# Performance work log

Measured on AMD Instinct MI355X. Metric: run time of the kernel, lower is better.

## Reference

```python
import jax, jax.numpy as jnp
import numpy as np

N = 100000
E = 1600000
IN_C = 128
HID = 64
HEADS = 2
OUT_C = 64
Z = 16
NEG_SLOPE = 0.2


def _gat_layer(x, src, dst, W, a_src, a_dst, b, heads, d):
    # x: [N, in], W: [in, heads*d]
    h = (x @ W).reshape(-1, heads, d)                      # [N, H, d]
    alpha_s = (h * a_src).sum(-1)                          # [N, H]
    alpha_d = (h * a_dst).sum(-1)                          # [N, H]
    e = jax.nn.leaky_relu(alpha_s[src] + alpha_d[dst], NEG_SLOPE)  # [E, H]
    m = jax.ops.segment_max(e, dst, num_segments=N)        # [N, H]
    ex = jnp.exp(e - m[dst])
    denom = jax.ops.segment_sum(ex, dst, num_segments=N)   # [N, H]
    alpha = ex / (denom[dst] + 1e-16)                      # [E, H]
    out = jax.ops.segment_sum(h[src] * alpha[:, :, None], dst, num_segments=N)  # [N, H, d]
    return out.reshape(-1, heads * d) + b


def setup_inputs() -> dict:
    key = jax.random.key(0)
    ks = jax.random.split(key, 24)
    g = lambda k, shp, fan: jax.random.normal(k, shp, jnp.float32) * (1.0 / np.sqrt(fan))
    inp = {
        "x": jax.random.normal(ks[0], (N, IN_C), jnp.float32),
        "edge_index": jax.random.randint(ks[1], (2, E), 0, N, jnp.int64),
        "edge_attr": jax.random.normal(ks[2], (E, 8), jnp.float32),
        "eps": jax.random.normal(ks[3], (N, Z), jnp.float32),
        # GAT layer 1: heads=2, d=HID
        "W1": g(ks[4], (IN_C, HEADS * HID), IN_C),
        "a_src1": g(ks[5], (HEADS, HID), HID),
        "a_dst1": g(ks[6], (HEADS, HID), HID),
        "b1": jnp.zeros((HEADS * HID,), jnp.float32),
        # GAT layer 2: heads=1, d=OUT_C
        "W2": g(ks[7], (HEADS * HID, OUT_C), HEADS * HID),
        "a_src2": g(ks[8], (1, OUT_C), OUT_C),
        "a_dst2": g(ks[9], (1, OUT_C), OUT_C),
        "b2": jnp.zeros((OUT_C,), jnp.float32),
        # VAE
        "fc1_w": g(ks[10], (64, 128), 64), "fc1_b": jnp.zeros((128,), jnp.float32),
        "mu_w": g(ks[11], (128, Z), 128), "mu_b": jnp.zeros((Z,), jnp.float32),
        "lv_w": g(ks[12], (128, Z), 128), "lv_b": jnp.zeros((Z,), jnp.float32),
        "fc3_w": g(ks[13], (Z, 128), Z), "fc3_b": jnp.zeros((128,), jnp.float32),
        "fc4_w": g(ks[14], (128, 64), 128), "fc4_b": jnp.zeros((64,), jnp.float32),
    }
    return inp


def reference(x, edge_index, edge_attr, eps, W1, a_src1, a_dst1, b1, W2, a_src2, a_dst2, b2,
              fc1_w, fc1_b, mu_w, mu_b, lv_w, lv_b, fc3_w, fc3_b, fc4_w, fc4_b):
    src, dst = edge_index[0], edge_index[1]
    # GAT stack (edge_attr ignored: GATConv edge_dim=None)
    h = jax.nn.relu(_gat_layer(x, src, dst, W1, a_src1, a_dst1, b1, HEADS, HID))
    gat_out = _gat_layer(h, src, dst, W2, a_src2, a_dst2, b2, 1, OUT_C)  # [N, 64]
    # VAE
    h1 = jax.nn.relu(gat_out @ fc1_w + fc1_b)
    mu = h1 @ mu_w + mu_b
    logvar = h1 @ lv_w + lv_b
    lv = jnp.clip(logvar, -10.0, 10.0)
    z = mu + eps * jnp.exp(0.5 * lv)
    h3 = jax.nn.relu(z @ fc3_w + fc3_b)
    recon = h3 @ fc4_w + fc4_b
    return recon, mu, logvar, gat_out
```

## Files before the change

kernel.cpp:

```cpp
#include <hip/hip_runtime.h>
#include <hip/hip_bf16.h>

__device__ __forceinline__ float4 fma4(float s, float4 b, float4 c) {
    c.x = fmaf(s, b.x, c.x); c.y = fmaf(s, b.y, c.y);
    c.z = fmaf(s, b.z, c.z); c.w = fmaf(s, b.w, c.w);
    return c;
}

__device__ __forceinline__ unsigned short f2b_bits(float x) {
    __hip_bfloat16 h = __float2bfloat16(x);
    unsigned short u;
    __builtin_memcpy(&u, &h, 2);
    return u;
}
__device__ __forceinline__ unsigned int pack2(float a, float b) {
    return (unsigned int)f2b_bits(a) | ((unsigned int)f2b_bits(b) << 16);
}
__device__ __forceinline__ float blo(unsigned int u) { return __uint_as_float(u << 16); }
__device__ __forceinline__ float bhi(unsigned int u) { return __uint_as_float(u & 0xffff0000u); }
__device__ __forceinline__ float sx8(unsigned int w, int b) {
    return (float)((int)(w << (24 - 8 * b)) >> 24);
}

template<int FIN, int FOUT, int BK, int ACT, int OUTK, bool ABF, int HD>
__global__ __launch_bounds__(256) void tgemm_k(const void* __restrict__ Av,
                                               const float* __restrict__ W,
                                               const float* __restrict__ bias,
                                               void* __restrict__ outv,
                                               float* __restrict__ scales,
                                               const float* __restrict__ asr,
                                               const float* __restrict__ adr,
                                               float* __restrict__ aso,
                                               float* __restrict__ ado, int n)
{
    constexpr int BM  = 128;
    constexpr int BMp = BM + 4;
    constexpr int NT_N = FOUT / 4;
    constexpr int NT_M = 256 / NT_N;
    constexpr int RG   = (BM / NT_M) / 4;
    __shared__ __align__(16) float As[BK * BMp];
    __shared__ __align__(16) float Bs[BK * FOUT];

    const float* Af = (const float*)Av;
    const unsigned short* Ab = (const unsigned short*)Av;

    const int t  = threadIdx.x;
    const int m0 = blockIdx.x * BM;
    const int tn = t % NT_N, tm = t / NT_N;

    float4 acc[RG][4];
    #pragma unroll
    for (int g = 0; g < RG; ++g)
        #pragma unroll
        for (int i = 0; i < 4; ++i) acc[g][i] = make_float4(0.f, 0.f, 0.f, 0.f);

    for (int kt = 0; kt < FIN; kt += BK) {
        __syncthreads();
        #pragma unroll
        for (int idx = t; idx < BM * BK / 4; idx += 256) {
            int r  = idx / (BK / 4);
            int c4 = (idx % (BK / 4)) * 4;
            int row = m0 + r;
            float4 v = make_float4(0.f, 0.f, 0.f, 0.f);
            if (row < n) {
                if constexpr (ABF) {
                    uint2 rv = *(const uint2*)(Ab + (size_t)row * FIN + kt + c4);
                    v = make_float4(blo(rv.x), bhi(rv.x), blo(rv.y), bhi(rv.y));
                } else {
                    v = *(const float4*)(Af + (size_t)row * FIN + kt + c4);
                }
            }
            As[(c4 + 0) * BMp + r] = v.x;
            As[(c4 + 1) * BMp + r] = v.y;
            As[(c4 + 2) * BMp + r] = v.z;
            As[(c4 + 3) * BMp + r] = v.w;
        }
        #pragma unroll
        for (int idx = t; idx < BK * FOUT / 4; idx += 256) {
            int kr = idx / (FOUT / 4);
            int c4 = (idx % (FOUT / 4)) * 4;
            *(float4*)(Bs + kr * FOUT + c4) =
                *(const float4*)(W + (size_t)(kt + kr) * FOUT + c4);
        }
        __syncthreads();
        #pragma unroll 8
        for (int k = 0; k < BK; ++k) {
            float4 b = *(const float4*)(Bs + k * FOUT + 4 * tn);
            #pragma unroll
            for (int g = 0; g < RG; ++g) {
                float4 a = *(const float4*)(As + k * BMp + 4 * (tm + NT_M * g));
                acc[g][0] = fma4(a.x, b, acc[g][0]);
                acc[g][1] = fma4(a.y, b, acc[g][1]);
                acc[g][2] = fma4(a.z, b, acc[g][2]);
                acc[g][3] = fma4(a.w, b, acc[g][3]);
            }
        }
    }

    if constexpr (HD > 0) {
        float4 av = *(const float4*)(asr + 4 * tn);
        float4 dv = *(const float4*)(adr + 4 * tn);
        const int head = tn / (NT_N / HD);
        #pragma unroll
        for (int g = 0; g < RG; ++g)
            #pragma unroll
            for (int i = 0; i < 4; ++i) {
                float4 o = acc[g][i];
                float ds = fmaf(o.x, av.x, fmaf(o.y, av.y, fmaf(o.z, av.z, o.w * av.w)));
                float dd = fmaf(o.x, dv.x, fmaf(o.y, dv.y, fmaf(o.z, dv.z, o.w * dv.w)));
                #pragma unroll
                for (int off = 8; off > 0; off >>= 1) {
                    ds += __shfl_xor(ds, off, 16);
                    dd += __shfl_xor(dd, off, 16);
                }
                if ((tn & 15) == 0) {
                    int row = m0 + 4 * (tm + NT_M * g) + i;
                    if (row < n) {
                        aso[(size_t)row * HD + head] = ds;
                        ado[(size_t)row * HD + head] = dd;
                    }
                }
            }
    }

    float4 bb = make_float4(0.f, 0.f, 0.f, 0.f);
    if (bias) bb = *(const float4*)(bias + 4 * tn);
    #pragma unroll
    for (int g = 0; g < RG; ++g)
        #pragma unroll
        for (int i = 0; i < 4; ++i) {
            int row = m0 + 4 * (tm + NT_M * g) + i;
            if (row < n) {
                float4 o = acc[g][i];
                if constexpr (OUTK == 2) {
                    float amax = fmaxf(fmaxf(fabsf(o.x), fabsf(o.y)),
                                       fmaxf(fabsf(o.z), fabsf(o.w)));
                    #pragma unroll
                    for (int off = NT_N / 2; off > 0; off >>= 1)
                        amax = fmaxf(amax, __shfl_xor(amax, off, NT_N));
                    float invsc = amax > 0.f ? 127.f / amax : 0.f;
                    int q0 = __float2int_rn(o.x * invsc);
                    int q1 = __float2int_rn(o.y * invsc);
                    int q2 = __float2int_rn(o.z * invsc);
                    int q3 = __float2int_rn(o.w * invsc);
                    unsigned int pv = (q0 & 255) | ((q1 & 255) << 8) |
                                      ((q2 & 255) << 16) | ((q3 & 255) << 24);
                    ((unsigned int*)outv)[(size_t)row * (FOUT / 4) + tn] = pv;
                    if (tn == 0) scales[row] = amax * (1.f / 127.f);
                } else {
                    o.x += bb.x; o.y += bb.y; o.z += bb.z; o.w += bb.w;
                    if (ACT == 1) {
                        o.x = fmaxf(o.x, 0.f); o.y = fmaxf(o.y, 0.f);
                        o.z = fmaxf(o.z, 0.f); o.w = fmaxf(o.w, 0.f);
                    }
                    if constexpr (OUTK == 1) {
                        unsigned short* outb = (unsigned short*)outv;
                        uint2 pv = make_uint2(pack2(o.x, o.y), pack2(o.z, o.w));
                        *(uint2*)(outb + (size_t)row * FOUT + 4 * tn) = pv;
                    } else {
                        float* outf = (float*)outv;
                        *(float4*)(outf + (size_t)row * FOUT + 4 * tn) = o;
                    }
                }
            }
        }
}

__global__ __launch_bounds__(256) void mulv_k(const float* __restrict__ A,
                                              const float* __restrict__ muw,
                                              const float* __restrict__ lvw,
                                              const float* __restrict__ mub,
                                              const float* __restrict__ lvb,
                                              const float* __restrict__ eps,
                                              float* __restrict__ o_mu,
                                              float* __restrict__ o_lv,
                                              float* __restrict__ zb, int n)
{
    constexpr int FIN = 128, BK = 32, BN = 32;
    constexpr int BM = 128, BMp = BM + 4;
    constexpr int NT_N = BN / 4;
    __shared__ __align__(16) float As[BK * BMp];
    __shared__ __align__(16) float Bs[BK * BN];

    const int t  = threadIdx.x;
    const int m0 = blockIdx.x * BM;
    const int tn = t % NT_N, tm = t / NT_N;

    float4 acc[4];
    #pragma unroll
    for (int i = 0; i < 4; ++i) acc[i] = make_float4(0.f, 0.f, 0.f, 0.f);

    for (int kt = 0; kt < FIN; kt += BK) {
        __syncthreads();
        #pragma unroll
        for (int idx = t; idx < BM * BK / 4; idx += 256) {
            int r  = idx / (BK / 4);
            int c4 = (idx % (BK / 4)) * 4;
            int row = m0 + r;
            float4 v = make_float4(0.f, 0.f, 0.f, 0.f);
            if (row < n) v = *(const float4*)(A + (size_t)row * FIN + kt + c4);
            As[(c4 + 0) * BMp + r] = v.x;
            As[(c4 + 1) * BMp + r] = v.y;
            As[(c4 + 2) * BMp + r] = v.z;
            As[(c4 + 3) * BMp + r] = v.w;
        }
        {
            int kr = t / 8, c4 = (t % 8) * 4;
            const float* src = (c4 < 16) ? (muw + (size_t)(kt + kr) * 16 + c4)
                                         : (lvw + (size_t)(kt + kr) * 16 + (c4 - 16));
            *(float4*)(Bs + kr * BN + c4) = *(const float4*)src;
        }
        __syncthreads();
        #pragma unroll 8
        for (int k = 0; k < BK; ++k) {
            float4 b = *(const float4*)(Bs + k * BN + 4 * tn);
            float4 a = *(const float4*)(As + k * BMp + 4 * tm);
            acc[0] = fma4(a.x, b, acc[0]);
            acc[1] = fma4(a.y, b, acc[1]);
            acc[2] = fma4(a.z, b, acc[2]);
            acc[3] = fma4(a.w, b, acc[3]);
        }
    }

    const bool is_mu = (tn < 4);
    const int  c16   = is_mu ? 4 * tn : 4 * tn - 16;
    float4 bb = is_mu ? *(const float4*)(mub + c16) : *(const float4*)(lvb + c16);

    #pragma unroll
    for (int i = 0; i < 4; ++i) {
        int row = m0 + 4 * tm + i;
        float4 v = acc[i];
        v.x += bb.x; v.y += bb.y; v.z += bb.z; v.w += bb.w;
        float4 lvx;
        lvx.x = __shfl_xor(v.x, 4, 64);
        lvx.y = __shfl_xor(v.y, 4, 64);
        lvx.z = __shfl_xor(v.z, 4, 64);
        lvx.w = __shfl_xor(v.w, 4, 64);
        if (row < n) {
            if (is_mu) {
                *(float4*)(o_mu + (size_t)row * 16 + c16) = v;
                float4 ep = *(const float4*)(eps + (size_t)row * 16 + c16);
                float4 z;
                z.x = fmaf(ep.x, __expf(0.5f * fminf(fmaxf(lvx.x, -10.f), 10.f)), v.x);
                z.y = fmaf(ep.y, __expf(0.5f * fminf(fmaxf(lvx.y, -10.f), 10.f)), v.y);
                z.z = fmaf(ep.z, __expf(0.5f * fminf(fmaxf(lvx.z, -10.f), 10.f)), v.z);
                z.w = fmaf(ep.w, __expf(0.5f * fminf(fmaxf(lvx.w, -10.f), 10.f)), v.w);
                *(float4*)(zb + (size_t)row * 16 + c16) = z;
            } else {
                *(float4*)(o_lv + (size_t)row * 16 + c16) = v;
            }
        }
    }
}

__global__ __launch_bounds__(256) void count_k(const int* __restrict__ ei, int* __restrict__ deg, int E)
{
    int e = blockIdx.x * 256 + threadIdx.x;
    if (e >= E) return;
    atomicAdd(&deg[ei[E + e]], 1);
}

__global__ __launch_bounds__(256) void scanA_k(const int* __restrict__ deg, int* __restrict__ incl,
                                               int* __restrict__ bsum, int n)
{
    __shared__ int sh[256];
    int i = blockIdx.x * 256 + threadIdx.x;
    int v = (i < n) ? deg[i] : 0;
    sh[threadIdx.x] = v;
    __syncthreads();
    #pragma unroll
    for (int o = 1; o < 256; o <<= 1) {
        int t = (threadIdx.x >= o) ? sh[threadIdx.x - o] : 0;
        __syncthreads();
        sh[threadIdx.x] += t;
        __syncthreads();
    }
    if (i < n) incl[i] = sh[threadIdx.x];
    if (threadIdx.x == 255) bsum[blockIdx.x] = sh[255];
}

__global__ __launch_bounds__(512) void scanB_k(int* __restrict__ bsum, int nb)
{
    __shared__ int sh[512];
    int v = (threadIdx.x < nb) ? bsum[threadIdx.x] : 0;
    sh[threadIdx.x] = v;
    __syncthreads();
    #pragma unroll
    for (int o = 1; o < 512; o <<= 1) {
        int t = (threadIdx.x >= o) ? sh[threadIdx.x - o] : 0;
        __syncthreads();
        sh[threadIdx.x] += t;
        __syncthreads();
    }
    if (threadIdx.x < nb) bsum[threadIdx.x] = sh[threadIdx.x] - v;
}

__global__ __launch_bounds__(256) void scanC_k(const int* __restrict__ deg, const int* __restrict__ incl,
                                               const int* __restrict__ bsum, int* __restrict__ off,
                                               int* __restrict__ cursor, int n, int E)
{
    int i = blockIdx.x * 256 + threadIdx.x;
    if (i >= n) return;
    int v = incl[i] - deg[i] + bsum[i >> 8];
    off[i] = v;
    cursor[i] = v;
    if (i == 0) off[n] = E;
}

__global__ __launch_bounds__(256) void scatter_k(const int* __restrict__ ei, int* __restrict__ cursor,
                                                 int* __restrict__ csr_src, int E, int n)
{
    const int grp = blockIdx.x & 7;
    const int bin = blockIdx.x >> 3;
    const int bpg = gridDim.x >> 3;
    const int rsz = (n + 7) >> 3;
    const int lo = grp * rsz;
    const int hi = min(n, lo + rsz);
    const int stride = bpg * 256;
    for (int e = bin * 256 + threadIdx.x; e < E; e += stride) {
        int d = ei[E + e];
        if (d >= lo && d < hi) {
            int pos = atomicAdd(&cursor[d], 1);
            csr_src[pos] = ei[e];
        }
    }
}

template<int FEAT, int H, int ACT, bool OUTB>
__global__ __launch_bounds__(256) void gat_agg_k(const int* __restrict__ csr_src,
                                                 const int* __restrict__ off,
                                                 const float* __restrict__ as_,
                                                 const float* __restrict__ ad_,
                                                 const unsigned int* __restrict__ h8,
                                                 const float* __restrict__ sc,
                                                 const float* __restrict__ bias,
                                                 void* __restrict__ outv, int n)
{
    constexpr int LANES = 16;
    constexpr int FPL   = FEAT / LANES;
    constexpr int WPR   = FEAT / 4;
    constexpr int SUBL  = LANES / H;
    constexpr int NCH   = 4;
    const int tid = blockIdx.x * 256 + threadIdx.x;
    const int d = tid >> 4;
    if (d >= n) return;
    const int lane = threadIdx.x & 15;
    const int myhead = lane / SUBL;
    const int sl = lane % SUBL;
    const int start = off[d], end = off[d + 1];
    const float adm = ad_[d * H + myhead];

    float vreg[NCH], sreg_sc[NCH]; int sreg[NCH];
    float m = -3.4e38f;
    #pragma unroll
    for (int c = 0; c < NCH; ++c) {
        int j = start + sl + c * SUBL;
        int s = 0; float v = -3.4e38f, scl = 0.f;
        if (j < end) {
            s = csr_src[j];
            v = as_[s * H + myhead] + adm;
            v = v > 0.f ? v : 0.2f * v;
            scl = sc[s];
        }
        sreg[c] = s; vreg[c] = v; sreg_sc[c] = scl;
        m = fmaxf(m, v);
    }
    for (int j = start + sl + NCH * SUBL; j < end; j += SUBL) {
        int s = csr_src[j];
        float v = as_[s * H + myhead] + adm;
        v = v > 0.f ? v : 0.2f * v;
        m = fmaxf(m, v);
    }
    #pragma unroll
    for (int o = SUBL / 2; o > 0; o >>= 1)
        m = fmaxf(m, __shfl_xor(m, o, SUBL));

    float ssum = 0.f;
    #pragma unroll
    for (int c = 0; c < NCH; ++c)
        if (start + sl + c * SUBL < end) ssum += __expf(vreg[c] - m);
    for (int j = start + sl + NCH * SUBL; j < end; j += SUBL) {
        int s = csr_src[j];
        float v = as_[s * H + myhead] + adm;
        v = v > 0.f ? v : 0.2f * v;
        ssum += __expf(v - m);
    }
    #pragma unroll
    for (int o = SUBL / 2; o > 0; o >>= 1)
        ssum += __shfl_xor(ssum, o, SUBL);
    const float inv = 1.f / (ssum + 1e-16f);

    float acc[FPL];
    #pragma unroll
    for (int k = 0; k < FPL; ++k) acc[k] = 0.f;

    auto body = [&](float a, int s) {
        if constexpr (FPL == 8) {
            uint2 r = ((const uint2*)(h8 + (size_t)s * WPR))[lane];
            acc[0] = fmaf(sx8(r.x, 0), a, acc[0]);
            acc[1] = fmaf(sx8(r.x, 1), a, acc[1]);
            acc[2] = fmaf(sx8(r.x, 2), a, acc[2]);
            acc[3] = fmaf(sx8(r.x, 3), a, acc[3]);
            acc[4] = fmaf(sx8(r.y, 0), a, acc[4]);
            acc[5] = fmaf(sx8(r.y, 1), a, acc[5]);
            acc[6] = fmaf(sx8(r.y, 2), a, acc[6]);
            acc[7] = fmaf(sx8(r.y, 3), a, acc[7]);
        } else {
            unsigned int r = (h8 + (size_t)s * WPR)[lane];
            acc[0] = fmaf(sx8(r, 0), a, acc[0]);
            acc[1] = fmaf(sx8(r, 1), a, acc[1]);
            acc[2] = fmaf(sx8(r, 2), a, acc[2]);
            acc[3] = fmaf(sx8(r, 3), a, acc[3]);
        }
    };

    const int nch = (end - start + SUBL - 1) / SUBL;
    for (int c = 0; c < nch; ++c) {
        const int j0 = start + c * SUBL;
        const int cnt = min(SUBL, end - j0);
        float myalpha = 0.f; int mysrc = 0;
        if (c < NCH) {
            mysrc = sreg[c];
            if (sl < cnt) myalpha = __expf(vreg[c] - m) * inv * sreg_sc[c];
        } else {
            if (sl < cnt) {
                mysrc = csr_src[j0 + sl];
                float v = as_[mysrc * H + myhead] + adm;
                v = v > 0.f ? v : 0.2f * v;
                myalpha = __expf(v - m) * inv * sc[mysrc];
            }
        }
        if (cnt == SUBL) {
            #pragma unroll
            for (int u = 0; u < SUBL; ++u) {
                float a = __shfl(myalpha, myhead * SUBL + u, LANES);
                int   s = __shfl(mysrc, u, LANES);
                body(a, s);
            }
        } else {
            for (int u = 0; u < cnt; ++u) {
                float a = __shfl(myalpha, myhead * SUBL + u, LANES);
                int   s = __shfl(mysrc, u, LANES);
                body(a, s);
            }
        }
    }

    if constexpr (OUTB) {
        float o[FPL];
        #pragma unroll
        for (int k = 0; k < FPL; ++k) {
            o[k] = acc[k] + bias[lane * FPL + k];
            if (ACT == 1) o[k] = fmaxf(o[k], 0.f);
        }
        uint4 pv;
        pv.x = pack2(o[0], o[1]); pv.y = pack2(o[2], o[3]);
        pv.z = pack2(o[4], o[5]); pv.w = pack2(o[6], o[7]);
        *(uint4*)((unsigned short*)outv + (size_t)d * FEAT + lane * FPL) = pv;
    } else {
        float* outf = (float*)outv;
        #pragma unroll
        for (int k = 0; k < FPL; ++k) {
            float o = acc[k] + bias[lane * FPL + k];
            if (ACT == 1) o = fmaxf(o, 0.f);
            outf[(size_t)d * FEAT + lane * FPL + k] = o;
        }
    }
}

extern "C" void kernel_launch(void* const* d_in, const int* in_sizes, int n_in,
                              void* d_out, int out_size, void* d_ws, size_t ws_size,
                              hipStream_t stream)
{
    const int n = in_sizes[0] / 128;
    const int E = in_sizes[1] / 2;

    const float* x   = (const float*)d_in[0];
    const int*   ei  = (const int*)d_in[1];
    const float* eps = (const float*)d_in[3];
    const float* W1  = (const float*)d_in[4];
    const float* as1w= (const float*)d_in[5];
    const float* ad1w= (const float*)d_in[6];
    const float* b1  = (const float*)d_in[7];
    const float* W2  = (const float*)d_in[8];
    const float* as2w= (const float*)d_in[9];
    const float* ad2w= (const float*)d_in[10];
    const float* b2  = (const float*)d_in[11];
    const float* fc1w= (const float*)d_in[12];
    const float* fc1b= (const float*)d_in[13];
    const float* muw = (const float*)d_in[14];
    const float* mub = (const float*)d_in[15];
    const float* lvw = (const float*)d_in[16];
    const float* lvb = (const float*)d_in[17];
    const float* fc3w= (const float*)d_in[18];
    const float* fc3b= (const float*)d_in[19];
    const float* fc4w= (const float*)d_in[20];
    const float* fc4b= (const float*)d_in[21];

    char* ws = (char*)d_ws;

    size_t oDeg   = 0;
    size_t oOff   = oDeg  + (size_t)n * 4;
    size_t oIncl  = oOff  + (size_t)(n + 1) * 4;
    size_t oCur   = oIncl + (size_t)n * 4;
    size_t oBsum  = oCur  + (size_t)n * 4;
    size_t oCsr   = oBsum + 512 * 4;
    size_t oH1    = oCsr  + (size_t)E * 4;
    size_t oHl2   = oH1   + (size_t)n * 128 * 4;
    size_t oH2    = oHl2  + (size_t)n * 128 * 4;
    size_t oAS1   = oH2   + (size_t)n * 64 * 4;
    size_t oAD1   = oAS1  + (size_t)n * 2 * 4;
    size_t oAS2   = oAD1  + (size_t)n * 2 * 4;
    size_t oAD2   = oAS2  + (size_t)n * 4;
    size_t oSC1   = oAD2  + (size_t)n * 4;
    size_t oSC2   = oSC1  + (size_t)n * 4;

    int* deg    = (int*)(ws + oDeg);
    int* off    = (int*)(ws + oOff);
    int* incl   = (int*)(ws + oIncl);
    int* cursor = (int*)(ws + oCur);
    int* bsum   = (int*)(ws + oBsum);
    int* csr    = (int*)(ws + oCsr);
    unsigned int* h1q = (unsigned int*)(ws + oH1);
    unsigned short* hl2b = (unsigned short*)(ws + oHl2);
    unsigned int* h2q = (unsigned int*)(ws + oH2);
    float* as1  = (float*)(ws + oAS1);
    float* ad1  = (float*)(ws + oAD1);
    float* as2  = (float*)(ws + oAS2);
    float* ad2  = (float*)(ws + oAD2);
    float* sc1  = (float*)(ws + oSC1);
    float* sc2  = (float*)(ws + oSC2);
    float* h1v  = (float*)(ws + oH1);
    float* h3   = (float*)(ws + oH1);
    float* zb   = (float*)(ws + oH2);

    float* out     = (float*)d_out;
    float* o_recon = out;
    float* o_mu    = out + (size_t)n * 64;
    float* o_lv    = out + (size_t)n * 80;
    float* o_gat   = out + (size_t)n * 96;

    const int ebl  = (E + 255) / 256;
    const int nbS  = (n + 255) / 256;
    const int abl  = (n * 16 + 255) / 256;
    const int gblk = (n + 127) / 128;

    hipMemsetAsync(deg, 0, (size_t)n * 4, stream);
    count_k<<<ebl, 256, 0, stream>>>(ei, deg, E);
    scanA_k<<<nbS, 256, 0, stream>>>(deg, incl, bsum, n);
    scanB_k<<<1, 512, 0, stream>>>(bsum, nbS);
    scanC_k<<<nbS, 256, 0, stream>>>(deg, incl, bsum, off, cursor, n, E);
    scatter_k<<<1024, 256, 0, stream>>>(ei, cursor, csr, E, n);

    tgemm_k<128, 128, 32, 0, 2, false, 2><<<gblk, 256, 0, stream>>>(
        x, W1, nullptr, h1q, sc1, as1w, ad1w, as1, ad1, n);
    gat_agg_k<128, 2, 1, true><<<abl, 256, 0, stream>>>(
        csr, off, as1, ad1, h1q, sc1, b1, hl2b, n);

    tgemm_k<128, 64, 32, 0, 2, true, 1><<<gblk, 256, 0, stream>>>(
        hl2b, W2, nullptr, h2q, sc2, as2w, ad2w, as2, ad2, n);
    gat_agg_k<64, 1, 0, false><<<abl, 256, 0, stream>>>(
        csr, off, as2, ad2, h2q, sc2, b2, o_gat, n);

    tgemm_k<64, 128, 32, 1, 0, false, 0><<<gblk, 256, 0, stream>>>(
        o_gat, fc1w, fc1b, h1v, nullptr, nullptr, nullptr, nullptr, nullptr, n);
    mulv_k<<<gblk, 256, 0, stream>>>(h1v, muw, lvw, mub, lvb, eps, o_mu, o_lv, zb, n);
    tgemm_k<16, 128, 16, 1, 0, false, 0><<<gblk, 256, 0, stream>>>(
        zb, fc3w, fc3b, h3, nullptr, nullptr, nullptr, nullptr, nullptr, n);
    tgemm_k<128, 64, 32, 0, 0, false, 0><<<gblk, 256, 0, stream>>>(
        h3, fc4w, fc4b, o_recon, nullptr, nullptr, nullptr, nullptr, nullptr, n);
}
```

Measured before the change: 525.9 us.

## Replace FP32 SIMT GEMMs with bf16 MFMA kernels and bf16 intermediates

Replaces the scalar-FMA tiled GEMM kernels (including the mu/logvar kernel) with one templated kernel that converts inputs and weights to bf16 in shared memory and uses 16x16x32 bf16 MFMA instructions. Per-row epilogues for attention logits and int8 quantization, bias/ReLU, and the reparameterization step are reworked for the MFMA output layout. VAE intermediates (h1, z, h3) are now stored as bf16, roughly halving their memory traffic. This trades precision on the dense layers, and per-block weight transposition overhead, for matrix-core throughput.

```diff
diff --git a/kernel.cpp b/kernel.cpp
--- a/kernel.cpp
+++ b/kernel.cpp
@@ -1,11 +1,8 @@
 #include <hip/hip_runtime.h>
 #include <hip/hip_bf16.h>
 
-__device__ __forceinline__ float4 fma4(float s, float4 b, float4 c) {
-    c.x = fmaf(s, b.x, c.x); c.y = fmaf(s, b.y, c.y);
-    c.z = fmaf(s, b.z, c.z); c.w = fmaf(s, b.w, c.w);
-    return c;
-}
+typedef __attribute__((ext_vector_type(8))) short bf16x8;
+typedef __attribute__((ext_vector_type(4))) float f32x4;
 
 __device__ __forceinline__ unsigned short f2b_bits(float x) {
     __hip_bfloat16 h = __float2bfloat16(x);
@@ -16,239 +13,181 @@
 __device__ __forceinline__ unsigned int pack2(float a, float b) {
     return (unsigned int)f2b_bits(a) | ((unsigned int)f2b_bits(b) << 16);
 }
-__device__ __forceinline__ float blo(unsigned int u) { return __uint_as_float(u << 16); }
-__device__ __forceinline__ float bhi(unsigned int u) { return __uint_as_float(u & 0xffff0000u); }
 __device__ __forceinline__ float sx8(unsigned int w, int b) {
     return (float)((int)(w << (24 - 8 * b)) >> 24);
 }
 
-template<int FIN, int FOUT, int BK, int ACT, int OUTK, bool ABF, int HD>
-__global__ __launch_bounds__(256) void tgemm_k(const void* __restrict__ Av,
-                                               const float* __restrict__ W,
-                                               const float* __restrict__ bias,
-                                               void* __restrict__ outv,
-                                               float* __restrict__ scales,
-                                               const float* __restrict__ asr,
-                                               const float* __restrict__ adr,
-                                               float* __restrict__ aso,
-                                               float* __restrict__ ado, int n)
-{
-    constexpr int BM  = 128;
-    constexpr int BMp = BM + 4;
-    constexpr int NT_N = FOUT / 4;
-    constexpr int NT_M = 256 / NT_N;
-    constexpr int RG   = (BM / NT_M) / 4;
-    __shared__ __align__(16) float As[BK * BMp];
-    __shared__ __align__(16) float Bs[BK * FOUT];
-
-    const float* Af = (const float*)Av;
-    const unsigned short* Ab = (const unsigned short*)Av;
+template<int FIN, int FOUT, int EPI, int HD, bool ABF, int ACT>
+__global__ __launch_bounds__(256) void mfma_k(const void* __restrict__ Av,
+                                              const float* __restrict__ W,
+                                              const float* __restrict__ W2,
+                                              const float* __restrict__ bias,
+                                              const float* __restrict__ bias2,
+                                              void* __restrict__ outv,
+                                              void* __restrict__ out2,
+                                              void* __restrict__ out3,
+                                              float* __restrict__ scales,
+                                              const float* __restrict__ asr,
+                                              const float* __restrict__ adr,
+                                              float* __restrict__ aso,
+                                              float* __restrict__ ado,
+                                              const float* __restrict__ epsp,
+                                              int n)
+{
+    constexpr int KE = (FIN < 32) ? 32 : FIN;
+    constexpr int KP = KE + 8;
+    constexpr int KS = KE / 32;
+    constexpr int NT = FOUT / 16;
+    __shared__ __align__(16) unsigned short As[64 * KP];
+    __shared__ __align__(16) unsigned short Wt[FOUT * KP];
 
     const int t  = threadIdx.x;
-    const int m0 = blockIdx.x * BM;
-    const int tn = t % NT_N, tm = t / NT_N;
-
-    float4 acc[RG][4];
-    #pragma unroll
-    for (int g = 0; g < RG; ++g)
-        #pragma unroll
-        for (int i = 0; i < 4; ++i) acc[g][i] = make_float4(0.f, 0.f, 0.f, 0.f);
-
-    for (int kt = 0; kt < FIN; kt += BK) {
-        __syncthreads();
-        #pragma unroll
-        for (int idx = t; idx < BM * BK / 4; idx += 256) {
-            int r  = idx / (BK / 4);
-            int c4 = (idx % (BK / 4)) * 4;
-            int row = m0 + r;
-            float4 v = make_float4(0.f, 0.f, 0.f, 0.f);
-            if (row < n) {
-                if constexpr (ABF) {
-                    uint2 rv = *(const uint2*)(Ab + (size_t)row * FIN + kt + c4);
-                    v = make_float4(blo(rv.x), bhi(rv.x), blo(rv.y), bhi(rv.y));
+    const int m0 = blockIdx.x * 64;
+
+    for (int idx = t; idx < 64 * (KE / 4); idx += 256) {
+        int r  = idx / (KE / 4);
+        int c4 = (idx % (KE / 4)) * 4;
+        int row = m0 + r;
+        unsigned int p0 = 0, p1 = 0;
+        if (row < n && c4 < FIN) {
+            if constexpr (ABF) {
+                uint2 rv = *(const uint2*)((const unsigned short*)Av + (size_t)row * FIN + c4);
+                p0 = rv.x; p1 = rv.y;
+            } else {
+                float4 v = *(const float4*)((const float*)Av + (size_t)row * FIN + c4);
+                p0 = pack2(v.x, v.y); p1 = pack2(v.z, v.w);
+            }
+        }
+        *(uint2*)(As + r * KP + c4) = make_uint2(p0, p1);
+    }
+    for (int idx = t; idx < KE * (FOUT / 4); idx += 256) {
+        int k  = idx / (FOUT / 4);
+        int c4 = (idx % (FOUT / 4)) * 4;
+        float4 v = make_float4(0.f, 0.f, 0.f, 0.f);
+        if (k < FIN) {
+            if constexpr (EPI == 3) {
+                v = (c4 < 16) ? *(const float4*)(W  + (size_t)k * 16 + c4)
+                              : *(const float4*)(W2 + (size_t)k * 16 + (c4 - 16));
+            } else {
+                v = *(const float4*)(W + (size_t)k * FOUT + c4);
+            }
+        }
+        Wt[(c4 + 0) * KP + k] = f2b_bits(v.x);
+        Wt[(c4 + 1) * KP + k] = f2b_bits(v.y);
+        Wt[(c4 + 2) * KP + k] = f2b_bits(v.z);
+        Wt[(c4 + 3) * KP + k] = f2b_bits(v.w);
+    }
+    __syncthreads();
+
+    const int w   = t >> 6;
+    const int l   = t & 63;
+    const int l15 = l & 15;
+    const int g   = l >> 4;
+    const int node = m0 + w * 16 + l15;
+
+    f32x4 acc[NT];
+    #pragma unroll
+    for (int i = 0; i < NT; ++i) acc[i] = (f32x4){0.f, 0.f, 0.f, 0.f};
+
+    #pragma unroll
+    for (int ks = 0; ks < KS; ++ks) {
+        bf16x8 nf = *(const bf16x8*)(As + (w * 16 + l15) * KP + ks * 32 + g * 8);
+        #pragma unroll
+        for (int tt = 0; tt < NT; ++tt) {
+            bf16x8 wf = *(const bf16x8*)(Wt + (tt * 16 + l15) * KP + ks * 32 + g * 8);
+            acc[tt] = __builtin_amdgcn_mfma_f32_16x16x32_bf16(wf, nf, acc[tt], 0, 0, 0);
+        }
+    }
+
+    if constexpr (EPI == 0 || EPI == 1) {
+        #pragma unroll
+        for (int tt = 0; tt < NT; ++tt) {
+            float4 bb = *(const float4*)(bias + 16 * tt + 4 * g);
+            float o0 = acc[tt][0] + bb.x, o1 = acc[tt][1] + bb.y;
+            float o2 = acc[tt][2] + bb.z, o3 = acc[tt][3] + bb.w;
+            if (ACT == 1) {
+                o0 = fmaxf(o0, 0.f); o1 = fmaxf(o1, 0.f);
+                o2 = fmaxf(o2, 0.f); o3 = fmaxf(o3, 0.f);
+            }
+            if (node < n) {
+                if constexpr (EPI == 0) {
+                    *(float4*)((float*)outv + (size_t)node * FOUT + 16 * tt + 4 * g) =
+                        make_float4(o0, o1, o2, o3);
                 } else {
-                    v = *(const float4*)(Af + (size_t)row * FIN + kt + c4);
+                    *(uint2*)((unsigned short*)outv + (size_t)node * FOUT + 16 * tt + 4 * g) =
+                        make_uint2(pack2(o0, o1), pack2(o2, o3));
                 }
             }
-            As[(c4 + 0) * BMp + r] = v.x;
-            As[(c4 + 1) * BMp + r] = v.y;
-            As[(c4 + 2) * BMp + r] = v.z;
-            As[(c4 + 3) * BMp + r] = v.w;
-        }
-        #pragma unroll
-        for (int idx = t; idx < BK * FOUT / 4; idx += 256) {
-            int kr = idx / (FOUT / 4);
-            int c4 = (idx % (FOUT / 4)) * 4;
-            *(float4*)(Bs + kr * FOUT + c4) =
-                *(const float4*)(W + (size_t)(kt + kr) * FOUT + c4);
-        }
-        __syncthreads();
-        #pragma unroll 8
-        for (int k = 0; k < BK; ++k) {
-            float4 b = *(const float4*)(Bs + k * FOUT + 4 * tn);
+        }
+    } else if constexpr (EPI == 2) {
+        float amax = 0.f;
+        float dsh[HD], ddh[HD];
+        #pragma unroll
+        for (int h = 0; h < HD; ++h) { dsh[h] = 0.f; ddh[h] = 0.f; }
+        #pragma unroll
+        for (int tt = 0; tt < NT; ++tt) {
+            float4 av = *(const float4*)(asr + 16 * tt + 4 * g);
+            float4 dv = *(const float4*)(adr + 16 * tt + 4 * g);
+            const float* avp = (const float*)&av;
+            const float* dvp = (const float*)&dv;
+            constexpr int TPH = NT;
+            const int h = (HD == 2) ? (tt / (NT / 2)) : 0;
             #pragma unroll
-            for (int g = 0; g < RG; ++g) {
-                float4 a = *(const float4*)(As + k * BMp + 4 * (tm + NT_M * g));
-                acc[g][0] = fma4(a.x, b, acc[g][0]);
-                acc[g][1] = fma4(a.y, b, acc[g][1]);
-                acc[g][2] = fma4(a.z, b, acc[g][2]);
-                acc[g][3] = fma4(a.w, b, acc[g][3]);
-            }
-        }
-    }
-
-    if constexpr (HD > 0) {
-        float4 av = *(const float4*)(asr + 4 * tn);
-        float4 dv = *(const float4*)(adr + 4 * tn);
-        const int head = tn / (NT_N / HD);
-        #pragma unroll
-        for (int g = 0; g < RG; ++g)
+            for (int j = 0; j < 4; ++j) {
+                float xv = acc[tt][j];
+                amax = fmaxf(amax, fabsf(xv));
+                dsh[h] = fmaf(xv, avp[j], dsh[h]);
+                ddh[h] = fmaf(xv, dvp[j], ddh[h]);
+            }
+            (void)TPH;
+        }
+        amax = fmaxf(amax, __shfl_xor(amax, 16, 64));
+        amax = fmaxf(amax, __shfl_xor(amax, 32, 64));
+        #pragma unroll
+        for (int h = 0; h < HD; ++h) {
+            dsh[h] += __shfl_xor(dsh[h], 16, 64);
+            dsh[h] += __shfl_xor(dsh[h], 32, 64);
+            ddh[h] += __shfl_xor(ddh[h], 16, 64);
+            ddh[h] += __shfl_xor(ddh[h], 32, 64);
+        }
+        float invsc = amax > 0.f ? 127.f / amax : 0.f;
+        if (node < n) {
             #pragma unroll
-            for (int i = 0; i < 4; ++i) {
-                float4 o = acc[g][i];
-                float ds = fmaf(o.x, av.x, fmaf(o.y, av.y, fmaf(o.z, av.z, o.w * av.w)));
-                float dd = fmaf(o.x, dv.x, fmaf(o.y, dv.y, fmaf(o.z, dv.z, o.w * dv.w)));
+            for (int tt = 0; tt < NT; ++tt) {
+                int q0 = __float2int_rn(acc[tt][0] * invsc);
+                int q1 = __float2int_rn(acc[tt][1] * invsc);
+                int q2 = __float2int_rn(acc[tt][2] * invsc);
+                int q3 = __float2int_rn(acc[tt][3] * invsc);
+                unsigned int pv = (q0 & 255) | ((q1 & 255) << 8) |
+                                  ((q2 & 255) << 16) | ((q3 & 255) << 24);
+                ((unsigned int*)outv)[(size_t)node * (FOUT / 4) + 4 * tt + g] = pv;
+            }
+            if (g == 0) {
+                scales[node] = amax * (1.f / 127.f);
                 #pragma unroll
-                for (int off = 8; off > 0; off >>= 1) {
-                    ds += __shfl_xor(ds, off, 16);
-                    dd += __shfl_xor(dd, off, 16);
+                for (int h = 0; h < HD; ++h) {
+                    aso[(size_t)node * HD + h] = dsh[h];
+                    ado[(size_t)node * HD + h] = ddh[h];
                 }
-                if ((tn & 15) == 0) {
-                    int row = m0 + 4 * (tm + NT_M * g) + i;
-                    if (row < n) {
-                        aso[(size_t)row * HD + head] = ds;
-                        ado[(size_t)row * HD + head] = dd;
-                    }
-                }
-            }
-    }
-
-    float4 bb = make_float4(0.f, 0.f, 0.f, 0.f);
-    if (bias) bb = *(const float4*)(bias + 4 * tn);
-    #pragma unroll
-    for (int g = 0; g < RG; ++g)
-        #pragma unroll
-        for (int i = 0; i < 4; ++i) {
-            int row = m0 + 4 * (tm + NT_M * g) + i;
-            if (row < n) {
-                float4 o = acc[g][i];
-                if constexpr (OUTK == 2) {
-                    float amax = fmaxf(fmaxf(fabsf(o.x), fabsf(o.y)),
-                                       fmaxf(fabsf(o.z), fabsf(o.w)));
-                    #pragma unroll
-                    for (int off = NT_N / 2; off > 0; off >>= 1)
-                        amax = fmaxf(amax, __shfl_xor(amax, off, NT_N));
-                    float invsc = amax > 0.f ? 127.f / amax : 0.f;
-                    int q0 = __float2int_rn(o.x * invsc);
-                    int q1 = __float2int_rn(o.y * invsc);
-                    int q2 = __float2int_rn(o.z * invsc);
-                    int q3 = __float2int_rn(o.w * invsc);
-                    unsigned int pv = (q0 & 255) | ((q1 & 255) << 8) |
-                                      ((q2 & 255) << 16) | ((q3 & 255) << 24);
-                    ((unsigned int*)outv)[(size_t)row * (FOUT / 4) + tn] = pv;
-                    if (tn == 0) scales[row] = amax * (1.f / 127.f);
-                } else {
-                    o.x += bb.x; o.y += bb.y; o.z += bb.z; o.w += bb.w;
-                    if (ACT == 1) {
-                        o.x = fmaxf(o.x, 0.f); o.y = fmaxf(o.y, 0.f);
-                        o.z = fmaxf(o.z, 0.f); o.w = fmaxf(o.w, 0.f);
-                    }
-                    if constexpr (OUTK == 1) {
-                        unsigned short* outb = (unsigned short*)outv;
-                        uint2 pv = make_uint2(pack2(o.x, o.y), pack2(o.z, o.w));
-                        *(uint2*)(outb + (size_t)row * FOUT + 4 * tn) = pv;
-                    } else {
-                        float* outf = (float*)outv;
-                        *(float4*)(outf + (size_t)row * FOUT + 4 * tn) = o;
-                    }
-                }
-            }
-        }
-}
-
-__global__ __launch_bounds__(256) void mulv_k(const float* __restrict__ A,
-                                              const float* __restrict__ muw,
-                                              const float* __restrict__ lvw,
-                                              const float* __restrict__ mub,
-                                              const float* __restrict__ lvb,
-                                              const float* __restrict__ eps,
-                                              float* __restrict__ o_mu,
-                                              float* __restrict__ o_lv,
-                                              float* __restrict__ zb, int n)
-{
-    constexpr int FIN = 128, BK = 32, BN = 32;
-    constexpr int BM = 128, BMp = BM + 4;
-    constexpr int NT_N = BN / 4;
-    __shared__ __align__(16) float As[BK * BMp];
-    __shared__ __align__(16) float Bs[BK * BN];
-
-    const int t  = threadIdx.x;
-    const int m0 = blockIdx.x * BM;
-    const int tn = t % NT_N, tm = t / NT_N;
-
-    float4 acc[4];
-    #pragma unroll
-    for (int i = 0; i < 4; ++i) acc[i] = make_float4(0.f, 0.f, 0.f, 0.f);
-
-    for (int kt = 0; kt < FIN; kt += BK) {
-        __syncthreads();
-        #pragma unroll
-        for (int idx = t; idx < BM * BK / 4; idx += 256) {
-            int r  = idx / (BK / 4);
-            int c4 = (idx % (BK / 4)) * 4;
-            int row = m0 + r;
-            float4 v = make_float4(0.f, 0.f, 0.f, 0.f);
-            if (row < n) v = *(const float4*)(A + (size_t)row * FIN + kt + c4);
-            As[(c4 + 0) * BMp + r] = v.x;
-            As[(c4 + 1) * BMp + r] = v.y;
-            As[(c4 + 2) * BMp + r] = v.z;
-            As[(c4 + 3) * BMp + r] = v.w;
-        }
-        {
-            int kr = t / 8, c4 = (t % 8) * 4;
-            const float* src = (c4 < 16) ? (muw + (size_t)(kt + kr) * 16 + c4)
-                                         : (lvw + (size_t)(kt + kr) * 16 + (c4 - 16));
-            *(float4*)(Bs + kr * BN + c4) = *(const float4*)src;
-        }
-        __syncthreads();
-        #pragma unroll 8
-        for (int k = 0; k < BK; ++k) {
-            float4 b = *(const float4*)(Bs + k * BN + 4 * tn);
-            float4 a = *(const float4*)(As + k * BMp + 4 * tm);
-            acc[0] = fma4(a.x, b, acc[0]);
-            acc[1] = fma4(a.y, b, acc[1]);
-            acc[2] = fma4(a.z, b, acc[2]);
-            acc[3] = fma4(a.w, b, acc[3]);
-        }
-    }
-
-    const bool is_mu = (tn < 4);
-    const int  c16   = is_mu ? 4 * tn : 4 * tn - 16;
-    float4 bb = is_mu ? *(const float4*)(mub + c16) : *(const float4*)(lvb + c16);
-
-    #pragma unroll
-    for (int i = 0; i < 4; ++i) {
-        int row = m0 + 4 * tm + i;
-        float4 v = acc[i];
-        v.x += bb.x; v.y += bb.y; v.z += bb.z; v.w += bb.w;
-        float4 lvx;
-        lvx.x = __shfl_xor(v.x, 4, 64);
-        lvx.y = __shfl_xor(v.y, 4, 64);
-        lvx.z = __shfl_xor(v.z, 4, 64);
-        lvx.w = __shfl_xor(v.w, 4, 64);
-        if (row < n) {
-            if (is_mu) {
-                *(float4*)(o_mu + (size_t)row * 16 + c16) = v;
-                float4 ep = *(const float4*)(eps + (size_t)row * 16 + c16);
-                float4 z;
-                z.x = fmaf(ep.x, __expf(0.5f * fminf(fmaxf(lvx.x, -10.f), 10.f)), v.x);
-                z.y = fmaf(ep.y, __expf(0.5f * fminf(fmaxf(lvx.y, -10.f), 10.f)), v.y);
-                z.z = fmaf(ep.z, __expf(0.5f * fminf(fmaxf(lvx.z, -10.f), 10.f)), v.z);
-                z.w = fmaf(ep.w, __expf(0.5f * fminf(fmaxf(lvx.w, -10.f), 10.f)), v.w);
-                *(float4*)(zb + (size_t)row * 16 + c16) = z;
-            } else {
-                *(float4*)(o_lv + (size_t)row * 16 + c16) = v;
-            }
+            }
+        }
+    } else {
+        float4 mb = *(const float4*)(bias  + 4 * g);
+        float4 lb = *(const float4*)(bias2 + 4 * g);
+        float mu0 = acc[0][0] + mb.x, mu1 = acc[0][1] + mb.y;
+        float mu2 = acc[0][2] + mb.z, mu3 = acc[0][3] + mb.w;
+        float lv0 = acc[1][0] + lb.x, lv1 = acc[1][1] + lb.y;
+        float lv2 = acc[1][2] + lb.z, lv3 = acc[1][3] + lb.w;
+        if (node < n) {
+            float4 ep = *(const float4*)(epsp + (size_t)node * 16 + 4 * g);
+            float z0 = fmaf(ep.x, __expf(0.5f * fminf(fmaxf(lv0, -10.f), 10.f)), mu0);
+            float z1 = fmaf(ep.y, __expf(0.5f * fminf(fmaxf(lv1, -10.f), 10.f)), mu1);
+            float z2 = fmaf(ep.z, __expf(0.5f * fminf(fmaxf(lv2, -10.f), 10.f)), mu2);
+            float z3 = fmaf(ep.w, __expf(0.5f * fminf(fmaxf(lv3, -10.f), 10.f)), mu3);
+            *(float4*)((float*)outv + (size_t)node * 16 + 4 * g) = make_float4(mu0, mu1, mu2, mu3);
+            *(float4*)((float*)out2 + (size_t)node * 16 + 4 * g) = make_float4(lv0, lv1, lv2, lv3);
+            *(uint2*)((unsigned short*)out3 + (size_t)node * 16 + 4 * g) =
+                make_uint2(pack2(z0, z1), pack2(z2, z3));
         }
     }
 }
@@ -505,10 +444,10 @@
     size_t oCur   = oIncl + (size_t)n * 4;
     size_t oBsum  = oCur  + (size_t)n * 4;
     size_t oCsr   = oBsum + 512 * 4;
-    size_t oH1    = oCsr  + (size_t)E * 4;
-    size_t oHl2   = oH1   + (size_t)n * 128 * 4;
-    size_t oH2    = oHl2  + (size_t)n * 128 * 4;
-    size_t oAS1   = oH2   + (size_t)n * 64 * 4;
+    size_t oR1    = oCsr  + (size_t)E * 4;
+    size_t oR2    = oR1   + (size_t)n * 256;
+    size_t oR3    = oR2   + (size_t)n * 256;
+    size_t oAS1   = oR3   + (size_t)n * 128;
     size_t oAD1   = oAS1  + (size_t)n * 2 * 4;
     size_t oAS2   = oAD1  + (size_t)n * 2 * 4;
     size_t oAD2   = oAS2  + (size_t)n * 4;
@@ -521,18 +460,18 @@
     int* cursor = (int*)(ws + oCur);
     int* bsum   = (int*)(ws + oBsum);
     int* csr    = (int*)(ws + oCsr);
-    unsigned int* h1q = (unsigned int*)(ws + oH1);
-    unsigned short* hl2b = (unsigned short*)(ws + oHl2);
-    unsigned int* h2q = (unsigned int*)(ws + oH2);
+    unsigned int*   h1q  = (unsigned int*)(ws + oR1);
+    unsigned short* h1v  = (unsigned short*)(ws + oR1);
+    unsigned short* hl2b = (unsigned short*)(ws + oR2);
+    unsigned short* h3   = (unsigned short*)(ws + oR2);
+    unsigned int*   h2q  = (unsigned int*)(ws + oR3);
+    unsigned short* zb   = (unsigned short*)(ws + oR3);
     float* as1  = (float*)(ws + oAS1);
     float* ad1  = (float*)(ws + oAD1);
     float* as2  = (float*)(ws + oAS2);
     float* ad2  = (float*)(ws + oAD2);
     float* sc1  = (float*)(ws + oSC1);
     float* sc2  = (float*)(ws + oSC2);
-    float* h1v  = (float*)(ws + oH1);
-    float* h3   = (float*)(ws + oH1);
-    float* zb   = (float*)(ws + oH2);
 
     float* out     = (float*)d_out;
     float* o_recon = out;
@@ -543,7 +482,7 @@
     const int ebl  = (E + 255) / 256;
     const int nbS  = (n + 255) / 256;
     const int abl  = (n * 16 + 255) / 256;
-    const int gblk = (n + 127) / 128;
+    const int g64  = (n + 63) / 64;
 
     hipMemsetAsync(deg, 0, (size_t)n * 4, stream);
     count_k<<<ebl, 256, 0, stream>>>(ei, deg, E);
@@ -552,21 +491,28 @@
     scanC_k<<<nbS, 256, 0, stream>>>(deg, incl, bsum, off, cursor, n, E);
     scatter_k<<<1024, 256, 0, stream>>>(ei, cursor, csr, E, n);
 
-    tgemm_k<128, 128, 32, 0, 2, false, 2><<<gblk, 256, 0, stream>>>(
-        x, W1, nullptr, h1q, sc1, as1w, ad1w, as1, ad1, n);
+    mfma_k<128, 128, 2, 2, false, 0><<<g64, 256, 0, stream>>>(
+        x, W1, nullptr, nullptr, nullptr, h1q, nullptr, nullptr,
+        sc1, as1w, ad1w, as1, ad1, nullptr, n);
     gat_agg_k<128, 2, 1, true><<<abl, 256, 0, stream>>>(
         csr, off, as1, ad1, h1q, sc1, b1, hl2b, n);
 
-    tgemm_k<128, 64, 32, 0, 2, true, 1><<<gblk, 256, 0, stream>>>(
-        hl2b, W2, nullptr, h2q, sc2, as2w, ad2w, as2, ad2, n);
+    mfma_k<128, 64, 2, 1, true, 0><<<g64, 256, 0, stream>>>(
+        hl2b, W2, nullptr, nullptr, nullptr, h2q, nullptr, nullptr,
+        sc2, as2w, ad2w, as2, ad2, nullptr, n);
     gat_agg_k<64, 1, 0, false><<<abl, 256, 0, stream>>>(
         csr, off, as2, ad2, h2q, sc2, b2, o_gat, n);
 
-    tgemm_k<64, 128, 32, 1, 0, false, 0><<<gblk, 256, 0, stream>>>(
-        o_gat, fc1w, fc1b, h1v, nullptr, nullptr, nullptr, nullptr, nullptr, n);
-    mulv_k<<<gblk, 256, 0, stream>>>(h1v, muw, lvw, mub, lvb, eps, o_mu, o_lv, zb, n);
-    tgemm_k<16, 128, 16, 1, 0, false, 0><<<gblk, 256, 0, stream>>>(
-        zb, fc3w, fc3b, h3, nullptr, nullptr, nullptr, nullptr, nullptr, n);
-    tgemm_k<128, 64, 32, 0, 0, false, 0><<<gblk, 256, 0, stream>>>(
-        h3, fc4w, fc4b, o_recon, nullptr, nullptr, nullptr, nullptr, nullptr, n);
-}
+    mfma_k<64, 128, 1, 0, false, 1><<<g64, 256, 0, stream>>>(
+        o_gat, fc1w, nullptr, fc1b, nullptr, h1v, nullptr, nullptr,
+        nullptr, nullptr, nullptr, nullptr, nullptr, nullptr, n);
+    mfma_k<128, 32, 3, 0, true, 0><<<g64, 256, 0, stream>>>(
+        h1v, muw, lvw, mub, lvb, o_mu, o_lv, zb,
+        nullptr, nullptr, nullptr, nullptr, nullptr, eps, n);
+    mfma_k<16, 128, 1, 0, true, 1><<<g64, 256, 0, stream>>>(
+        zb, fc3w, nullptr, fc3b, nullptr, h3, nullptr, nullptr,
+        nullptr, nullptr, nullptr, nullptr, nullptr, nullptr, n);
+    mfma_k<128, 64, 0, 0, true, 0><<<g64, 256, 0, stream>>>(
+        h3, fc4w, nullptr, fc4b, nullptr, o_recon, nullptr, nullptr,
+        nullptr, nullptr, nullptr, nullptr, nullptr, nullptr, n);
+}
```

New measurement: 423.6 us. 19.5% less time.
